# Performance work log

Measured on AMD Instinct MI355X. Metric: run time of the kernel, lower is better.

The kernel has to match this reference:

```python
import jax, jax.numpy as jnp
import numpy as np

B = 32          # patients
D = 128         # hidden dim (modality_embedding_dim == total_hidden_dim)
H = 4           # attention heads
DH = D // H     # per-head dim
L = 2           # num_graph_layers
N = {'ct': 1024, 'pet': 1024, 'clin': 256, 'gen': 2048, 'pat': 1}
# (src_type, dst_type) for the 8 relation types registered in _setup_relations
REL = [('ct','ct'), ('pet','pet'), ('clin','clin'), ('gen','gen'),
       ('pat','clin'), ('ct','gen'), ('pet','gen'), ('gen','pat')]
E_REL = [8192, 8192, 2048, 16384, 256, 8192, 8192, 2048]
EDGE_NAMES = ['e_ct','e_pet','e_clin','e_gen','e_pat2clin','e_ct2gen','e_pet2gen','e_gen2pat']


def setup_inputs() -> dict:
    key = jax.random.key(0)
    ks = iter(jax.random.split(key, 64))
    nk = lambda: next(ks)
    inp = {}
    inp['x_ct']   = jax.random.normal(nk(), (B, N['ct'],  D), jnp.float32)
    inp['x_pet']  = jax.random.normal(nk(), (B, N['pet'], D), jnp.float32)
    inp['x_clin'] = jax.random.normal(nk(), (B, N['clin'],D), jnp.float32)
    inp['x_gen']  = jax.random.normal(nk(), (B, N['gen'], D), jnp.float32)
    inp['early']  = jax.random.normal(nk(), (B, D), jnp.float32)

    def mk_edges(k, E, ns, nd):
        k1, k2 = jax.random.split(k)
        src = jax.random.randint(k1, (B, 1, E), 0, ns, jnp.int32)
        dst = jax.random.randint(k2, (B, 1, E), 0, nd, jnp.int32)
        return jnp.concatenate([src, dst], axis=1)  # [B,2,E]

    for nm, (s, d), E in zip(EDGE_NAMES, REL, E_REL):
        inp[nm] = mk_edges(nk(), E, N[s], N[d])

    sw = 1.0 / np.sqrt(D)
    inp['W_src'] = jax.random.normal(nk(), (L, 8, D, D), jnp.float32) * sw
    inp['W_dst'] = jax.random.normal(nk(), (L, 8, D, D), jnp.float32) * sw
    inp['a_src'] = jax.random.normal(nk(), (L, 8, H, DH), jnp.float32) * sw
    inp['a_dst'] = jax.random.normal(nk(), (L, 8, H, DH), jnp.float32) * sw
    inp['Wp'] = jax.random.normal(nk(), (3, D, D), jnp.float32) * sw  # CT, PET, genomic pooling
    inp['bp'] = jnp.zeros((3, D), jnp.float32)
    inp['W_sem'] = jax.random.normal(nk(), (4 * D, 128), jnp.float32) * (1.0 / np.sqrt(4 * D))
    inp['b_sem'] = jnp.zeros((128,), jnp.float32)
    inp['q_sem'] = jax.random.normal(nk(), (128,), jnp.float32) * sw
    return inp


def _leaky_relu(x):
    return jnp.where(x > 0, x, 0.2 * x)


def _gat_layer(x, edges, Ws, Wd, As, Ad):
    """One heterogeneous multi-head GAT layer summing over relation types."""
    agg = {t: jnp.zeros((B, N[t], H, DH), jnp.float32) for t in N}
    for r, ((s, d), ei) in enumerate(zip(REL, edges)):
        hs = jnp.einsum('bnd,de->bne', x[s], Ws[r]).reshape(B, N[s], H, DH)
        hd = jnp.einsum('bnd,de->bne', x[d], Wd[r]).reshape(B, N[d], H, DH)
        al_s = jnp.sum(hs * As[r], axis=-1)  # [B,Ns,H]
        al_d = jnp.sum(hd * Ad[r], axis=-1)  # [B,Nd,H]
        nd = N[d]

        def one(hs_b, as_b, ad_b, e_b):
            src, dst = e_b[0], e_b[1]
            logit = _leaky_relu(as_b[src] + ad_b[dst])                      # [E,H]
            m = jnp.full((nd, H), -1e30, logit.dtype).at[dst].max(logit)    # segment max
            p = jnp.exp(logit - m[dst])
            den = jnp.zeros((nd, H), p.dtype).at[dst].add(p)
            w = p / (den[dst] + 1e-16)                                      # edge softmax per dst node
            msg = w[:, :, None] * hs_b[src]                                 # [E,H,DH]
            return jnp.zeros((nd, H, DH), msg.dtype).at[dst].add(msg)

        agg[d] = agg[d] + jax.vmap(one)(hs, al_s, al_d, ei)
    return {t: jax.nn.elu(agg[t].reshape(B, N[t], D)) for t in N}


def _pool(feat, W, b):
    # query = Linear(mean(features)); scores = feat @ q; softmax-weighted sum
    q = jnp.mean(feat, axis=1) @ W + b            # [B,D]
    sc = jnp.einsum('bnd,bd->bn', feat, q)        # [B,N]
    w = jax.nn.softmax(sc, axis=1)
    return jnp.einsum('bn,bnd->bd', w, feat)      # [B,D]


def _forward(x_ct, x_pet, x_clin, x_gen, early, edges,
             W_src, W_dst, a_src, a_dst, Wp, bp, W_sem, b_sem, q_sem):
    x = {'ct': x_ct, 'pet': x_pet, 'clin': x_clin, 'gen': x_gen,
         'pat': early[:, None, :]}
    for l in range(L):
        x = _gat_layer(x, edges, W_src[l], W_dst[l], a_src[l], a_dst[l])
    ct_p  = _pool(x['ct'],  Wp[0], bp[0])
    pet_p = _pool(x['pet'], Wp[1], bp[1])
    gen_p = _pool(x['gen'], Wp[2], bp[2])   # shared across the 3 meta-paths
    pad = jnp.zeros((B, 2 * D), ct_p.dtype)  # pad 2D -> 4D as in original
    imm = jnp.concatenate([ct_p, gen_p, pad], axis=1)
    pro = jnp.concatenate([pet_p, gen_p, pad], axis=1)
    trt = jnp.concatenate([(ct_p + pet_p) * 0.5, gen_p, pad], axis=1)
    z = jnp.stack([imm, pro, trt], axis=1)                     # [B,3,4D]
    s = jnp.einsum('bpa,a->bp', jnp.tanh(jnp.einsum('bpf,fa->bpa', z, W_sem) + b_sem), q_sem)
    beta = jax.nn.softmax(s, axis=1)                           # [B,3]
    fused = jnp.einsum('bp,bpf->bf', beta, z)                  # [B,4D]
    return fused, beta


def reference(x_ct, x_pet, x_clin, x_gen, early,
              e_ct, e_pet, e_clin, e_gen, e_pat2clin, e_ct2gen, e_pet2gen, e_gen2pat,
              W_src, W_dst, a_src, a_dst, Wp, bp, W_sem, b_sem, q_sem):
    edges = [e_ct, e_pet, e_clin, e_gen, e_pat2clin, e_ct2gen, e_pet2gen, e_gen2pat]
    return _forward(x_ct, x_pet, x_clin, x_gen, early, edges,
                    W_src, W_dst, a_src, a_dst, Wp, bp, W_sem, b_sem, q_sem)
```

## Files before the change

kernel.cpp:

```cpp
#include <hip/hip_runtime.h>
#include <math.h>

static constexpr int NB = 32;
static constexpr int ND = 128;

typedef short bf16x8 __attribute__((ext_vector_type(8)));
typedef float f32x4  __attribute__((ext_vector_type(4)));
typedef unsigned short u16x8 __attribute__((ext_vector_type(8)));

__device__ __forceinline__ float lrelu(float x){ return x > 0.f ? x : 0.2f*x; }
__device__ __forceinline__ unsigned short f2b(float f){
  unsigned u = __float_as_uint(f);
  return (unsigned short)((u + 0x7FFFu + ((u>>16)&1u)) >> 16);
}
__device__ __forceinline__ float b2f(unsigned short b){
  return __uint_as_float(((unsigned)b) << 16);
}

__global__ __launch_bounds__(128) void k_fold(const float* __restrict__ Wsrc,
    const float* __restrict__ Wdst, const float* __restrict__ asrc,
    const float* __restrict__ adst, float* __restrict__ vbuf){
  const int wid[5] = {0,1,3,5,6};
  int lr = blockIdx.x, role = blockIdx.y, l = blockIdx.z;
  int r = wid[lr];
  const float* W = (role ? Wdst : Wsrc) + (size_t)(l*8+r)*16384;
  const float* a = (role ? adst : asrc) + (size_t)(l*8+r)*128;
  int k = threadIdx.x;
  float* o = vbuf + ((size_t)((l*5+lr)*2+role))*512 + k*4;
  #pragma unroll
  for(int h=0;h<4;h++){
    float s = 0.f;
    #pragma unroll
    for(int j=0;j<32;j++) s += W[k*128 + h*32 + j]*a[h*32 + j];
    o[h] = s;
  }
}

__global__ __launch_bounds__(256) void k_wpack(const float* __restrict__ Wsrc,
    unsigned short* __restrict__ Wf){
  const int wid[5] = {0,1,3,5,6};
  int lr = blockIdx.x, l = blockIdx.y;
  const float* W = Wsrc + (size_t)(l*8+wid[lr])*16384;
  unsigned short* o = Wf + (size_t)((l*5+lr)*4)*4096;
  for(int idx=threadIdx.x; idx<128*128; idx+=256){
    int k = idx >> 7, col = idx & 127;
    int h = col >> 5, cc = col & 31;
    int k4 = k>>2, g = k4&3, kk = k4>>3, j = 4*((k4>>2)&1) + (k&3);
    int nb = cc>>4, lane = (cc&15) + 16*g;
    o[(size_t)h*4096 + ((size_t)((kk*2+nb)*64 + lane))*8 + j] = f2b(W[k*128 + col]);
  }
}

struct CsrP {
  const int* eg[5];
  int l2E[5];
  int Nd_[5];
  int roff_[5];
  int eoff_[5];
};

__global__ __launch_bounds__(512) void k_csr(CsrP P, int* __restrict__ rowstart,
                                             int* __restrict__ srcidx){
  int b = blockIdx.x, r = blockIdx.y, t = threadIdx.x;
  int E = 1<<P.l2E[r], Nd = P.Nd_[r];
  const int* eg = P.eg[r] + (size_t)b*2*E;
  int* rsO = rowstart + P.roff_[r] + b*(Nd+1);
  int* siO = srcidx + P.eoff_[r] + (size_t)b*E;
  __shared__ int cnt[2048];
  __shared__ int wsums[8];
  for(int i=t;i<Nd;i+=512) cnt[i]=0;
  __syncthreads();
  for(int e=t;e<E;e+=512) atomicAdd(&cnt[eg[E+e]], 1);
  __syncthreads();
  int C = Nd >> 9;
  int base = t*C;
  int loc[4]; int s_=0;
  for(int i=0;i<C;i++){ loc[i]=cnt[base+i]; s_+=loc[i]; }
  int lane = t&63, wv = t>>6;
  int sinc = s_;
  #pragma unroll
  for(int off=1;off<64;off<<=1){
    int u = __shfl_up(sinc, off);
    if(lane>=off) sinc += u;
  }
  if(lane==63) wsums[wv]=sinc;
  __syncthreads();
  int wbase=0, total=0;
  #pragma unroll
  for(int i=0;i<8;i++){ int v=wsums[i]; if(i<wv) wbase+=v; total+=v; }
  int excl = wbase + sinc - s_;
  for(int i=0;i<C;i++){
    int idx=base+i;
    rsO[idx]=excl; cnt[idx]=excl; excl+=loc[i];
  }
  if(t==0) rsO[Nd]=total;
  __syncthreads();
  for(int e=t;e<E;e+=512){
    int src=eg[e], dst=eg[E+e];
    int pos=atomicAdd(&cnt[dst],1);
    siO[pos]=src;
  }
}

struct HsP {
  int tb[4];
  int usef;
  const float* xf[3];
  unsigned long long xoff[3];
  int Ns[3];
  int nW[3];
  unsigned long long wfo[3][2];
  unsigned long long hso[3][2];
  unsigned long long aso[3][2];
  unsigned long long asrco[3][2];
  int nvd[3];
  unsigned long long vdo[3][3];
  unsigned long long aldo2[3][3];
  int ndd[3][3];
};

__global__ __launch_bounds__(256) void k_hs(HsP P, const unsigned short* __restrict__ x16,
    const unsigned short* __restrict__ Wf, const float* __restrict__ asrc,
    const float* __restrict__ vbuf, unsigned short* __restrict__ hs,
    float* __restrict__ als, float* __restrict__ ald){
  __shared__ unsigned short xl[16*132];
  int B = blockIdx.x;
  int t=0; while(t<2 && B>=P.tb[t+1]) t++;
  int local = B - P.tb[t];
  int b = local & 31, tile = local >> 5;
  int n0 = tile*16;
  int tid = threadIdx.x, w = tid>>6, ln = tid&63;
  if(P.usef){
    const float* xf = P.xf[t] + ((size_t)((size_t)b*P.Ns[t] + n0))*128;
    int row = tid>>4, c8 = tid&15;
    float4 a = *(const float4*)(xf + (size_t)row*128 + c8*8);
    float4 c = *(const float4*)(xf + (size_t)row*128 + c8*8 + 4);
    u16x8 r;
    r[0]=f2b(a.x); r[1]=f2b(a.y); r[2]=f2b(a.z); r[3]=f2b(a.w);
    r[4]=f2b(c.x); r[5]=f2b(c.y); r[6]=f2b(c.z); r[7]=f2b(c.w);
    *(u16x8*)&xl[row*132 + c8*8] = r;
  } else {
    int row = tid>>4, ch = tid&15;
    u16x8 v = *(const u16x8*)(x16 + P.xoff[t] + ((size_t)((size_t)b*P.Ns[t] + n0+row)*128 + ch*8));
    *(u16x8*)&xl[row*132 + ch*8] = v;
  }
  __syncthreads();
  int g = ln>>4, r15 = ln&15;
  for(int rep=0; rep<P.nW[t]; rep++){
    const unsigned short* wf = Wf + P.wfo[t][rep] + (size_t)w*4096;
    f32x4 acc[2]; acc[0]=(f32x4){0,0,0,0}; acc[1]=(f32x4){0,0,0,0};
    #pragma unroll
    for(int kk=0;kk<4;kk++){
      const unsigned short* pa = &xl[r15*132 + kk*32 + 4*g];
      ushort4 lo = *(const ushort4*)pa;
      ushort4 hi = *(const ushort4*)(pa+16);
      union { ushort u[8]; bf16x8 v; } tmp;
      tmp.u[0]=lo.x; tmp.u[1]=lo.y; tmp.u[2]=lo.z; tmp.u[3]=lo.w;
      tmp.u[4]=hi.x; tmp.u[5]=hi.y; tmp.u[6]=hi.z; tmp.u[7]=hi.w;
      bf16x8 af = tmp.v;
      #pragma unroll
      for(int nb=0;nb<2;nb++){
        bf16x8 bw = *(const bf16x8*)(wf + ((size_t)((kk*2+nb)*64 + ln))*8);
        acc[nb] = __builtin_amdgcn_mfma_f32_16x16x32_bf16(af, bw, acc[nb], 0, 0, 0);
      }
    }
    unsigned short* ho = hs + P.hso[t][rep] + ((size_t)b*P.Ns[t] + n0)*128;
    #pragma unroll
    for(int qq=0;qq<4;qq++){
      int m = 4*g + qq;
      #pragma unroll
      for(int nb=0;nb<2;nb++){
        ho[(size_t)m*128 + w*32 + nb*16 + r15] = f2b(acc[nb][qq]);
      }
    }
    {
      const float* aS = asrc + P.asrco[t][rep];
      float a0v = aS[w*32 + r15], a1v = aS[w*32 + 16 + r15];
      float p0 = acc[0][0]*a0v + acc[1][0]*a1v;
      float p1 = acc[0][1]*a0v + acc[1][1]*a1v;
      float p2 = acc[0][2]*a0v + acc[1][2]*a1v;
      float p3 = acc[0][3]*a0v + acc[1][3]*a1v;
      #pragma unroll
      for(int off=1; off<16; off<<=1){
        p0 += __shfl_xor(p0,off); p1 += __shfl_xor(p1,off);
        p2 += __shfl_xor(p2,off); p3 += __shfl_xor(p3,off);
      }
      if(r15 < 4){
        float pv = (r15==0)?p0:((r15==1)?p1:((r15==2)?p2:p3));
        als[P.aso[t][rep] + ((size_t)b*P.Ns[t] + n0 + 4*g + r15)*4 + w] = pv;
      }
    }
  }
  int nvd = P.nvd[t];
  if(tid < (nvd<<6)){
    int vd = tid>>6, rem = tid&63, row = rem>>2, h = rem&3;
    const float* vv = vbuf + P.vdo[t][vd];
    float s = 0.f;
    #pragma unroll 8
    for(int k=0;k<128;k++) s += b2f(xl[row*132+k]) * vv[k*4+h];
    ald[P.aldo2[t][vd] + ((size_t)b*P.ndd[t][vd] + n0 + row)*4 + h] = s;
  }
}

static constexpr int MAXE4 = 1536;
static constexpr int WST4  = 1548;

struct Fu5P {
  int nrel[3], ndshift[3];
  int roff[3][3], eoff[3][3], E[3][3], Ns[3][3];
  int rowbase[3][3];
  unsigned long long aldo[3][3];
  unsigned long long outoff[3];
};

__global__ __launch_bounds__(512, 8) void k_fuse6(Fu5P P,
    const int* __restrict__ rowstart, const int* __restrict__ srcidx,
    const float* __restrict__ als, const float* __restrict__ ald,
    const unsigned short* __restrict__ hs, unsigned short* __restrict__ out16){
  __shared__ float wlds[4*WST4];
  __shared__ int   silds[MAXE4];
  __shared__ int   rsl[3*65];
  int B = blockIdx.x;
  int xcd = B & 7, slot = B >> 3;
  int bg = slot >> 6, rem = slot & 63;
  int b = bg*8 + xcd;
  int t, dtile;
  if(rem < 32){ t = 0; dtile = rem; }
  else if(rem < 48){ t = 1; dtile = rem - 32; }
  else { t = 2; dtile = rem - 48; }
  int Nd = 1 << P.ndshift[t];
  int d0 = dtile * 64;
  int tid = threadIdx.x, w = tid>>6, ln = tid&63;
  int nrel = P.nrel[t];

  for(int q=0;q<nrel;q++){
    const int* rsq = rowstart + P.roff[t][q] + b*(Nd+1) + d0;
    for(int i=tid;i<65;i+=512) rsl[q*65+i] = rsq[i];
  }
  __syncthreads();

  for(int s=tid; s<(nrel<<8); s+=512){
    int q = s>>8, r2 = s&255, dloc = r2>>2, j = r2&3;
    int rs0 = rsl[q*65+dloc];
    int deg = rsl[q*65+dloc+1] - rs0;
    int cb = 0;
    for(int q2=0;q2<nrel;q2++) cb += rsl[q2*65+dloc] - rsl[q2*65];
    for(int q2=0;q2<q;q2++)    cb += rsl[q2*65+dloc+1] - rsl[q2*65+dloc];
    const int* si = srcidx + P.eoff[t][q] + (size_t)b*P.E[t][q];
    int bake = P.rowbase[t][q] + b*P.Ns[t][q];
    float4 ad4 = *(const float4*)(ald + P.aldo[t][q] + ((size_t)b*Nd + d0 + dloc)*4);
    float m0=-1e30f,m1=-1e30f,m2=-1e30f,m3=-1e30f;
    for(int i=j;i<deg;i+=4){
      int e = cb+i;
      int sil = bake + si[rs0+i];
      silds[e] = sil;
      float4 as4 = *(const float4*)(als + 4*(size_t)sil);
      float l0=lrelu(as4.x+ad4.x), l1=lrelu(as4.y+ad4.y);
      float l2=lrelu(as4.z+ad4.z), l3=lrelu(as4.w+ad4.w);
      wlds[0*WST4+e]=l0; wlds[1*WST4+e]=l1;
      wlds[2*WST4+e]=l2; wlds[3*WST4+e]=l3;
      m0=fmaxf(m0,l0); m1=fmaxf(m1,l1); m2=fmaxf(m2,l2); m3=fmaxf(m3,l3);
    }
    m0=fmaxf(m0,__shfl_xor(m0,1)); m1=fmaxf(m1,__shfl_xor(m1,1));
    m2=fmaxf(m2,__shfl_xor(m2,1)); m3=fmaxf(m3,__shfl_xor(m3,1));
    m0=fmaxf(m0,__shfl_xor(m0,2)); m1=fmaxf(m1,__shfl_xor(m1,2));
    m2=fmaxf(m2,__shfl_xor(m2,2)); m3=fmaxf(m3,__shfl_xor(m3,2));
    float n0_=0.f,n1_=0.f,n2_=0.f,n3_=0.f;
    for(int i=j;i<deg;i+=4){
      int e = cb+i;
      float p0=__expf(wlds[0*WST4+e]-m0); wlds[0*WST4+e]=p0; n0_+=p0;
      float p1=__expf(wlds[1*WST4+e]-m1); wlds[1*WST4+e]=p1; n1_+=p1;
      float p2=__expf(wlds[2*WST4+e]-m2); wlds[2*WST4+e]=p2; n2_+=p2;
      float p3=__expf(wlds[3*WST4+e]-m3); wlds[3*WST4+e]=p3; n3_+=p3;
    }
    n0_+=__shfl_xor(n0_,1); n1_+=__shfl_xor(n1_,1);
    n2_+=__shfl_xor(n2_,1); n3_+=__shfl_xor(n3_,1);
    n0_+=__shfl_xor(n0_,2); n1_+=__shfl_xor(n1_,2);
    n2_+=__shfl_xor(n2_,2); n3_+=__shfl_xor(n3_,2);
    float i0=1.f/(n0_+1e-16f), i1=1.f/(n1_+1e-16f);
    float i2=1.f/(n2_+1e-16f), i3=1.f/(n3_+1e-16f);
    for(int i=j;i<deg;i+=4){
      int e = cb+i;
      wlds[0*WST4+e]*=i0; wlds[1*WST4+e]*=i1;
      wlds[2*WST4+e]*=i2; wlds[3*WST4+e]*=i3;
    }
  }
  __syncthreads();

  int h = ln>>4;
  float accA[8], accB[8];
  #pragma unroll
  for(int i=0;i<8;i++){ accA[i]=0.f; accB[i]=0.f; }
  #pragma unroll
  for(int it=0; it<8; it++){
    int dloc = w*8 + it;
    int e0=0, e1=0;
    for(int q2=0;q2<nrel;q2++){
      int r0 = rsl[q2*65];
      e0 += rsl[q2*65+dloc]   - r0;
      e1 += rsl[q2*65+dloc+1] - r0;
    }
    float a0 = 0.f, a1 = 0.f;
    int e = e0;
    int eal = (e0+3)&~3; if(eal > e1) eal = e1;
    for(; e<eal; e++){
      float wv = wlds[h*WST4 + e];
      unsigned v = *(const unsigned*)(hs + ((size_t)silds[e]*128 + 2*ln));
      a0 += wv*__uint_as_float(v<<16);
      a1 += wv*__uint_as_float(v&0xFFFF0000u);
    }
    for(; e+8<=e1; e+=8){
      int4  sq0 = *(const int4*)&silds[e];
      int4  sq1 = *(const int4*)&silds[e+4];
      float4 wq0 = *(const float4*)&wlds[h*WST4 + e];
      float4 wq1 = *(const float4*)&wlds[h*WST4 + e + 4];
      unsigned v0 = *(const unsigned*)(hs + ((size_t)sq0.x*128 + 2*ln));
      unsigned v1 = *(const unsigned*)(hs + ((size_t)sq0.y*128 + 2*ln));
      unsigned v2 = *(const unsigned*)(hs + ((size_t)sq0.z*128 + 2*ln));
      unsigned v3 = *(const unsigned*)(hs + ((size_t)sq0.w*128 + 2*ln));
      unsigned v4 = *(const unsigned*)(hs + ((size_t)sq1.x*128 + 2*ln));
      unsigned v5 = *(const unsigned*)(hs + ((size_t)sq1.y*128 + 2*ln));
      unsigned v6 = *(const unsigned*)(hs + ((size_t)sq1.z*128 + 2*ln));
      unsigned v7 = *(const unsigned*)(hs + ((size_t)sq1.w*128 + 2*ln));
      a0 += wq0.x*__uint_as_float(v0<<16); a1 += wq0.x*__uint_as_float(v0&0xFFFF0000u);
      a0 += wq0.y*__uint_as_float(v1<<16); a1 += wq0.y*__uint_as_float(v1&0xFFFF0000u);
      a0 += wq0.z*__uint_as_float(v2<<16); a1 += wq0.z*__uint_as_float(v2&0xFFFF0000u);
      a0 += wq0.w*__uint_as_float(v3<<16); a1 += wq0.w*__uint_as_float(v3&0xFFFF0000u);
      a0 += wq1.x*__uint_as_float(v4<<16); a1 += wq1.x*__uint_as_float(v4&0xFFFF0000u);
      a0 += wq1.y*__uint_as_float(v5<<16); a1 += wq1.y*__uint_as_float(v5&0xFFFF0000u);
      a0 += wq1.z*__uint_as_float(v6<<16); a1 += wq1.z*__uint_as_float(v6&0xFFFF0000u);
      a0 += wq1.w*__uint_as_float(v7<<16); a1 += wq1.w*__uint_as_float(v7&0xFFFF0000u);
    }
    for(; e+4<=e1; e+=4){
      int4  sq = *(const int4*)&silds[e];
      float4 wq = *(const float4*)&wlds[h*WST4 + e];
      unsigned v0 = *(const unsigned*)(hs + ((size_t)sq.x*128 + 2*ln));
      unsigned v1 = *(const unsigned*)(hs + ((size_t)sq.y*128 + 2*ln));
      unsigned v2 = *(const unsigned*)(hs + ((size_t)sq.z*128 + 2*ln));
      unsigned v3 = *(const unsigned*)(hs + ((size_t)sq.w*128 + 2*ln));
      a0 += wq.x*__uint_as_float(v0<<16); a1 += wq.x*__uint_as_float(v0&0xFFFF0000u);
      a0 += wq.y*__uint_as_float(v1<<16); a1 += wq.y*__uint_as_float(v1&0xFFFF0000u);
      a0 += wq.z*__uint_as_float(v2<<16); a1 += wq.z*__uint_as_float(v2&0xFFFF0000u);
      a0 += wq.w*__uint_as_float(v3<<16); a1 += wq.w*__uint_as_float(v3&0xFFFF0000u);
    }
    for(; e<e1; e++){
      float wv = wlds[h*WST4 + e];
      unsigned v = *(const unsigned*)(hs + ((size_t)silds[e]*128 + 2*ln));
      a0 += wv*__uint_as_float(v<<16);
      a1 += wv*__uint_as_float(v&0xFFFF0000u);
    }
    accA[it] = a0; accB[it] = a1;
  }
  #pragma unroll
  for(int it=0; it<8; it++){
    int m = d0 + w*8 + it;
    float v0 = accA[it], v1 = accB[it];
    v0 = v0 > 0.f ? v0 : expm1f(v0);
    v1 = v1 > 0.f ? v1 : expm1f(v1);
    ushort2 o; o.x = f2b(v0); o.y = f2b(v1);
    *(ushort2*)(out16 + P.outoff[t] + ((size_t)b*Nd + m)*128 + 2*ln) = o;
  }
}

__device__ __constant__ const size_t POFF[3] = {0ull, 4194304ull, 8388608ull};
__device__ __constant__ const int    PNN[3]  = {1024, 1024, 2048};
static constexpr int PCH = 64;
static constexpr int MAXCH = 32;

__global__ __launch_bounds__(128) void k_pool_psum(const unsigned short* __restrict__ x2,
    float* __restrict__ part){
  int p = blockIdx.z, b = blockIdx.x, c = blockIdx.y, t = threadIdx.x;
  int Nn = PNN[p];
  if(c*PCH >= Nn) return;
  const unsigned short* f = x2 + POFF[p] + ((size_t)b*Nn + c*PCH)*ND;
  float acc = 0.f;
  #pragma unroll 8
  for(int n=0;n<PCH;n++) acc += b2f(f[(size_t)n*ND + t]);
  part[(((size_t)p*NB + b)*MAXCH + c)*ND + t] = acc;
}

__global__ __launch_bounds__(128) void k_pool_q(const float* __restrict__ part,
    const float* __restrict__ Wp, const float* __restrict__ bp,
    float* __restrict__ q){
  int p = blockIdx.z, b = blockIdx.x, t = threadIdx.x;
  int nch = PNN[p]/PCH;
  __shared__ float mean[ND];
  float s = 0.f;
  for(int c=0;c<nch;c++) s += part[(((size_t)p*NB + b)*MAXCH + c)*ND + t];
  mean[t] = s / (float)PNN[p];
  __syncthreads();
  const float* W = Wp + (size_t)p*ND*ND;
  float qv = bp[p*ND + t];
  #pragma unroll 8
  for(int k=0;k<ND;k++) qv += mean[k]*W[k*ND + t];
  q[((size_t)p*NB + b)*ND + t] = qv;
}

__global__ __launch_bounds__(256) void k_pool_score(const unsigned short* __restrict__ x2,
    const float* __restrict__ q, float* __restrict__ sc){
  int p = blockIdx.z, b = blockIdx.y;
  int w = threadIdx.x >> 6, lane = threadIdx.x & 63;
  int n = blockIdx.x*4 + w;
  int Nn = PNN[p];
  if(n >= Nn) return;
  const unsigned short* f  = x2 + POFF[p] + ((size_t)b*Nn + n)*ND;
  const float* qb = q + ((size_t)p*NB + b)*ND;
  float s = b2f(f[lane])*qb[lane] + b2f(f[lane+64])*qb[lane+64];
  #pragma unroll
  for(int off=32; off; off>>=1) s += __shfl_xor(s, off);
  if(lane == 0) sc[((size_t)p*NB + b)*2048 + n] = s;
}

__global__ __launch_bounds__(256) void k_pool_smax(const float* __restrict__ sc,
    float* __restrict__ stat){
  int p = blockIdx.z, b = blockIdx.x, t = threadIdx.x;
  int Nn = PNN[p];
  __shared__ float red[256];
  const float* s = sc + ((size_t)p*NB + b)*2048;
  float mx = -1e30f;
  for(int n=t;n<Nn;n+=256) mx = fmaxf(mx, s[n]);
  red[t] = mx; __syncthreads();
  for(int o=128;o;o>>=1){ if(t<o) red[t]=fmaxf(red[t],red[t+o]); __syncthreads(); }
  mx = red[0]; __syncthreads();
  float sum = 0.f;
  for(int n=t;n<Nn;n+=256) sum += __expf(s[n]-mx);
  red[t] = sum; __syncthreads();
  for(int o=128;o;o>>=1){ if(t<o) red[t]+=red[t+o]; __syncthreads(); }
  if(t==0){ stat[((size_t)p*NB + b)*2] = mx; stat[((size_t)p*NB + b)*2+1] = 1.f/red[0]; }
}

__global__ __launch_bounds__(128) void k_pool_wsum(const unsigned short* __restrict__ x2,
    const float* __restrict__ sc, const float* __restrict__ stat,
    float* __restrict__ part){
  int p = blockIdx.z, b = blockIdx.x, c = blockIdx.y, t = threadIdx.x;
  int Nn = PNN[p];
  if(c*PCH >= Nn) return;
  __shared__ float wsh[PCH];
  float mx  = stat[((size_t)p*NB + b)*2];
  float inv = stat[((size_t)p*NB + b)*2+1];
  if(t < PCH) wsh[t] = __expf(sc[((size_t)p*NB + b)*2048 + c*PCH + t] - mx)*inv;
  __syncthreads();
  const unsigned short* f = x2 + POFF[p] + ((size_t)b*Nn + c*PCH)*ND;
  float acc = 0.f;
  #pragma unroll 8
  for(int n=0;n<PCH;n++) acc += wsh[n]*b2f(f[(size_t)n*ND + t]);
  part[(((size_t)p*NB + b)*MAXCH + c)*ND + t] = acc;
}

__global__ __launch_bounds__(128) void k_pool_comb(const float* __restrict__ part,
    float* __restrict__ pooled){
  int p = blockIdx.z, b = blockIdx.x, t = threadIdx.x;
  int nch = PNN[p]/PCH;
  float s = 0.f;
  for(int c=0;c<nch;c++) s += part[(((size_t)p*NB + b)*MAXCH + c)*ND + t];
  pooled[((size_t)p*NB + b)*ND + t] = s;
}

__global__ __launch_bounds__(128) void k_sem(const float* __restrict__ ctp,
    const float* __restrict__ petp, const float* __restrict__ genp,
    const float* __restrict__ Wsem, const float* __restrict__ bsem,
    const float* __restrict__ qsem, float* __restrict__ fused, float* __restrict__ beta){
  int b = blockIdx.x, t = threadIdx.x;
  __shared__ float z[3][256];
  __shared__ float red[128];
  float ct = ctp[b*ND + t], pet = petp[b*ND + t], gen = genp[b*ND + t];
  z[0][t]=ct;  z[1][t]=pet; z[2][t]=0.5f*(ct+pet);
  z[0][ND+t]=gen; z[1][ND+t]=gen; z[2][ND+t]=gen;
  __syncthreads();
  float s[3];
  for(int p=0;p<3;p++){
    float a = bsem[t];
    for(int f=0;f<256;f++) a += z[p][f]*Wsem[f*128 + t];
    a = tanhf(a);
    red[t] = a * qsem[t];
    __syncthreads();
    for(int o=64;o>0;o>>=1){ if(t<o) red[t]+=red[t+o]; __syncthreads(); }
    s[p] = red[0]; __syncthreads();
  }
  float mx = fmaxf(s[0], fmaxf(s[1], s[2]));
  float e0 = __expf(s[0]-mx), e1 = __expf(s[1]-mx), e2 = __expf(s[2]-mx);
  float sm = e0+e1+e2;
  float b0 = e0/sm, b1 = e1/sm, b2 = e2/sm;
  if(t < 3) beta[b*3 + t] = (t==0)?b0:((t==1)?b1:b2);
  float f0 = b0*z[0][t] + b1*z[1][t] + b2*z[2][t];
  float f1 = b0*z[0][ND+t] + b1*z[1][ND+t] + b2*z[2][ND+t];
  fused[(size_t)b*512 + t]       = f0;
  fused[(size_t)b*512 + 128 + t] = f1;
  fused[(size_t)b*512 + 256 + t] = 0.f;
  fused[(size_t)b*512 + 384 + t] = 0.f;
}

extern "C" void kernel_launch(void* const* d_in, const int* in_sizes, int n_in,
                              void* d_out, int out_size, void* d_ws, size_t ws_size,
                              hipStream_t stream) {
  static const int wid[5]    = {0,1,3,5,6};
  static const int edgein[5] = {5,6,8,10,11};
  static const int l2E[5]    = {13,13,14,13,13};
  static const int Nd_l[5]   = {1024,1024,2048,2048,2048};
  static const int E_l[5]    = {8192,8192,16384,8192,8192};
  static const int Ns_l[5]   = {1024,1024,2048,1024,1024};
  static const int eoff[6]   = {0,262144,524288,1048576,1310720,1572864};
  static const int roff[5]   = {0,32800,65600,131168,196736};
  static const unsigned long long aoff[5]   = {0,131072,262144,524288,655360};
  static const unsigned long long aldoff[5] = {0,131072,262144,524288,786432};
  static const unsigned long long hsoff_lr[5] = {0ull,4194304ull,8388608ull,16777216ull,20971520ull};
  static const unsigned long long ALD = 786432;

  const float* Wsrc = (const float*)d_in[13];
  const float* Wp   = (const float*)d_in[17];
  const float* bp   = (const float*)d_in[18];
  const float* Wsem = (const float*)d_in[19];
  const float* bsem = (const float*)d_in[20];
  const float* qsem = (const float*)d_in[21];

  unsigned short* xc16 = (unsigned short*)d_ws;
  unsigned short* x2b16 = xc16;
  unsigned short* xmid16 = xc16 + 16777216;
  float* albase = (float*)(xmid16 + 16777216);
  float* als = albase;
  float* ald = albase + ALD;
  float* vbuf = albase + 1835008;
  unsigned short* wfbuf = (unsigned short*)(vbuf + 10240);
  float* pooled = (float*)(wfbuf + 163840);
  float* part = pooled + 12288;
  float* qbuf = part + 393216;
  float* scbuf = qbuf + 12288;
  float* stat = scbuf + 196608;
  int* rowstart = (int*)(stat + 192);
  int* srcidx = rowstart + 262304;
  unsigned short* hs16 = (unsigned short*)(srcidx + 1572864);

  { dim3 g(5,2,2); k_fold<<<g,128,0,stream>>>(Wsrc, (const float*)d_in[14],
                                              (const float*)d_in[15], (const float*)d_in[16], vbuf); }
  { dim3 g(5,2); k_wpack<<<g,256,0,stream>>>(Wsrc, wfbuf); }

  CsrP csr;
  for(int r=0;r<5;r++){
    csr.eg[r] = (const int*)d_in[edgein[r]];
    csr.l2E[r] = l2E[r]; csr.Nd_[r] = Nd_l[r];
    csr.roff_[r] = roff[r]; csr.eoff_[r] = eoff[r];
  }
  { dim3 g(NB,5); k_csr<<<g,512,0,stream>>>(csr, rowstart, srcidx); }

  static const unsigned long long xoo[3] = {0,4194304,8388608};
  static const int t2_nrel[3] = {3,1,1};
  static const int t2_lrel[3][3] = {{2,3,4},{0,0,0},{1,0,0}};
  static const int t2_nds[3] = {11,10,10};
  static const int t2_out[3] = {2,0,1};

  Fu5P fp;
  for(int t=0;t<3;t++){
    fp.nrel[t]=t2_nrel[t]; fp.ndshift[t]=t2_nds[t]; fp.outoff[t]=xoo[t2_out[t]];
    for(int q=0;q<3;q++){
      int lr = t2_lrel[t][q];
      fp.roff[t][q]=roff[lr]; fp.eoff[t][q]=eoff[lr];
      fp.E[t][q]=E_l[lr]; fp.Ns[t][q]=Ns_l[lr];
      fp.rowbase[t][q]=(int)(aoff[lr]/4);
      fp.aldo[t][q]=aldoff[lr];
    }
  }

  static const int hs_lr[3][2] = {{0,3},{1,4},{2,2}};
  static const int vd_lr[3][3] = {{0,0,0},{1,0,0},{2,3,4}};
  HsP hp;
  hp.tb[0]=0; hp.tb[1]=2048; hp.tb[2]=4096; hp.tb[3]=8192;
  hp.xf[0]=(const float*)d_in[0]; hp.xf[1]=(const float*)d_in[1]; hp.xf[2]=(const float*)d_in[3];
  hp.xoff[0]=0; hp.xoff[1]=4194304; hp.xoff[2]=8388608;
  hp.Ns[0]=1024; hp.Ns[1]=1024; hp.Ns[2]=2048;
  hp.nW[0]=2; hp.nW[1]=2; hp.nW[2]=1;
  hp.nvd[0]=1; hp.nvd[1]=1; hp.nvd[2]=3;
  for(int t=0;t<3;t++){
    for(int rep=0;rep<2;rep++){
      int lr = hs_lr[t][rep];
      hp.hso[t][rep]=hsoff_lr[lr];
      hp.aso[t][rep]=aoff[lr];
    }
    for(int vd=0;vd<3;vd++){
      int lr = vd_lr[t][vd];
      hp.aldo2[t][vd]=aldoff[lr];
      hp.ndd[t][vd]=Nd_l[lr];
    }
  }
  hp.hso[2][1]=0; hp.aso[2][1]=0;

  for(int l=0;l<2;l++){
    unsigned short* xout = (l==0) ? xmid16 : x2b16;
    hp.usef = (l==0) ? 1 : 0;

    for(int t=0;t<3;t++){
      for(int rep=0;rep<2;rep++){
        int lr = hs_lr[t][rep];
        hp.wfo[t][rep]=(unsigned long long)((l*5 + lr)*4)*4096;
        hp.asrco[t][rep]=(unsigned long long)((l*8 + wid[lr])*128);
      }
      for(int vd=0;vd<3;vd++){
        int lr = vd_lr[t][vd];
        hp.vdo[t][vd]=((unsigned long long)((l*5+lr)*2+1))*512;
      }
    }
    k_hs<<<8192,256,0,stream>>>(hp, xmid16, wfbuf, (const float*)d_in[15], vbuf,
                                hs16, als, ald);

    k_fuse6<<<2048,512,0,stream>>>(fp, rowstart, srcidx, als, ald, hs16, xout);
  }

  {
    dim3 gchunk(NB, MAXCH, 3);
    dim3 gone(NB, 1, 3);
    dim3 gscore(512, NB, 3);
    k_pool_psum <<<gchunk,128,0,stream>>>(x2b16, part);
    k_pool_q    <<<gone,  128,0,stream>>>(part, Wp, bp, qbuf);
    k_pool_score<<<gscore,256,0,stream>>>(x2b16, qbuf, scbuf);
    k_pool_smax <<<gone,  256,0,stream>>>(scbuf, stat);
    k_pool_wsum <<<gchunk,128,0,stream>>>(x2b16, scbuf, stat, part);
    k_pool_comb <<<gone,  128,0,stream>>>(part, pooled);
  }

  float* fused = (float*)d_out;
  float* beta  = fused + (size_t)NB*512;
  k_sem<<<NB,128,0,stream>>>(pooled, pooled + NB*ND, pooled + 2*NB*ND,
                             Wsem, bsem, qsem, fused, beta);
}
```

Baseline: 331.7 us.

## Make GAT aggregation wave-local with per-wave softmax and interleaved dst types

The fused edge-softmax/aggregation kernel now gives each wave its own 8 destination nodes with private LDS slices, replacing the block-wide rowstart staging and __syncthreads with wave-local shuffles and a wave barrier. The softmax drops max-subtraction and computes exp directly in one pass, removing two LDS passes. Node types are interleaved across waves within a block to balance load. It risks overflow without max-subtraction and fixed 240-edge per-wave buffers that could overflow for high-degree nodes.

```diff
diff --git a/kernel.cpp b/kernel.cpp
--- a/kernel.cpp
+++ b/kernel.cpp
@@ -202,8 +202,7 @@
   }
 }
 
-static constexpr int MAXE4 = 1536;
-static constexpr int WST4  = 1548;
+static constexpr int WSL = 240;
 
 struct Fu5P {
   int nrel[3], ndshift[3];
@@ -213,107 +212,105 @@
   unsigned long long outoff[3];
 };
 
-__global__ __launch_bounds__(512, 8) void k_fuse6(Fu5P P,
+__global__ __launch_bounds__(512, 8) void k_fuse7(Fu5P P,
     const int* __restrict__ rowstart, const int* __restrict__ srcidx,
     const float* __restrict__ als, const float* __restrict__ ald,
     const unsigned short* __restrict__ hs, unsigned short* __restrict__ out16){
-  __shared__ float wlds[4*WST4];
-  __shared__ int   silds[MAXE4];
-  __shared__ int   rsl[3*65];
+  __shared__ float wlds_all[8*4*WSL];
+  __shared__ int   silds_all[8*WSL];
   int B = blockIdx.x;
+  int w = threadIdx.x >> 6, ln = threadIdx.x & 63;
   int xcd = B & 7, slot = B >> 3;
   int bg = slot >> 6, rem = slot & 63;
   int b = bg*8 + xcd;
-  int t, dtile;
-  if(rem < 32){ t = 0; dtile = rem; }
-  else if(rem < 48){ t = 1; dtile = rem - 32; }
-  else { t = 2; dtile = rem - 48; }
+  int v = rem*8 + w;
+  int g = v >> 2, k4 = v & 3;
+  int t, tile;
+  if(k4 < 2){ t = 0; tile = g*2 + k4; }
+  else if(k4 == 2){ t = 1; tile = g; }
+  else { t = 2; tile = g; }
   int Nd = 1 << P.ndshift[t];
-  int d0 = dtile * 64;
-  int tid = threadIdx.x, w = tid>>6, ln = tid&63;
+  int d0 = tile * 8;
   int nrel = P.nrel[t];
-
-  for(int q=0;q<nrel;q++){
-    const int* rsq = rowstart + P.roff[t][q] + b*(Nd+1) + d0;
-    for(int i=tid;i<65;i+=512) rsl[q*65+i] = rsq[i];
-  }
-  __syncthreads();
-
-  for(int s=tid; s<(nrel<<8); s+=512){
-    int q = s>>8, r2 = s&255, dloc = r2>>2, j = r2&3;
-    int rs0 = rsl[q*65+dloc];
-    int deg = rsl[q*65+dloc+1] - rs0;
-    int cb = 0;
-    for(int q2=0;q2<nrel;q2++) cb += rsl[q2*65+dloc] - rsl[q2*65];
-    for(int q2=0;q2<q;q2++)    cb += rsl[q2*65+dloc+1] - rsl[q2*65+dloc];
-    const int* si = srcidx + P.eoff[t][q] + (size_t)b*P.E[t][q];
+  float* wlds = wlds_all + w*4*WSL;
+  int*  silds = silds_all + w*WSL;
+  int dst = ln >> 3, sub = ln & 7;
+  int d = d0 + dst;
+
+  int len0=0, len1=0, len2=0, s00=0, s01=0, s02=0;
+  {
+    const int* rsq = rowstart + P.roff[t][0] + b*(Nd+1);
+    s00 = rsq[d]; len0 = rsq[d+1] - s00;
+  }
+  if(nrel > 1){
+    const int* rsq1 = rowstart + P.roff[t][1] + b*(Nd+1);
+    s01 = rsq1[d]; len1 = rsq1[d+1] - s01;
+    const int* rsq2 = rowstart + P.roff[t][2] + b*(Nd+1);
+    s02 = rsq2[d]; len2 = rsq2[d+1] - s02;
+  }
+  int clen = len0 + len1 + len2;
+  int mybase = 0;
+  #pragma unroll
+  for(int dd=0; dd<7; dd++){
+    int vl = __shfl(clen, dd*8);
+    if(dd < dst) mybase += vl;
+  }
+
+  auto dorel = [&](int q, int s0q, int lq, int segb){
+    const int* si = srcidx + P.eoff[t][q] + (size_t)b*P.E[t][q] + s0q;
     int bake = P.rowbase[t][q] + b*P.Ns[t][q];
-    float4 ad4 = *(const float4*)(ald + P.aldo[t][q] + ((size_t)b*Nd + d0 + dloc)*4);
-    float m0=-1e30f,m1=-1e30f,m2=-1e30f,m3=-1e30f;
-    for(int i=j;i<deg;i+=4){
-      int e = cb+i;
-      int sil = bake + si[rs0+i];
+    float4 ad4 = *(const float4*)(ald + P.aldo[t][q] + ((size_t)b*Nd + d)*4);
+    float dn0=0.f, dn1=0.f, dn2=0.f, dn3=0.f;
+    for(int i=sub; i<lq; i+=8){
+      int e = segb + i;
+      int sil = bake + si[i];
       silds[e] = sil;
       float4 as4 = *(const float4*)(als + 4*(size_t)sil);
-      float l0=lrelu(as4.x+ad4.x), l1=lrelu(as4.y+ad4.y);
-      float l2=lrelu(as4.z+ad4.z), l3=lrelu(as4.w+ad4.w);
-      wlds[0*WST4+e]=l0; wlds[1*WST4+e]=l1;
-      wlds[2*WST4+e]=l2; wlds[3*WST4+e]=l3;
-      m0=fmaxf(m0,l0); m1=fmaxf(m1,l1); m2=fmaxf(m2,l2); m3=fmaxf(m3,l3);
-    }
-    m0=fmaxf(m0,__shfl_xor(m0,1)); m1=fmaxf(m1,__shfl_xor(m1,1));
-    m2=fmaxf(m2,__shfl_xor(m2,1)); m3=fmaxf(m3,__shfl_xor(m3,1));
-    m0=fmaxf(m0,__shfl_xor(m0,2)); m1=fmaxf(m1,__shfl_xor(m1,2));
-    m2=fmaxf(m2,__shfl_xor(m2,2)); m3=fmaxf(m3,__shfl_xor(m3,2));
-    float n0_=0.f,n1_=0.f,n2_=0.f,n3_=0.f;
-    for(int i=j;i<deg;i+=4){
-      int e = cb+i;
-      float p0=__expf(wlds[0*WST4+e]-m0); wlds[0*WST4+e]=p0; n0_+=p0;
-      float p1=__expf(wlds[1*WST4+e]-m1); wlds[1*WST4+e]=p1; n1_+=p1;
-      float p2=__expf(wlds[2*WST4+e]-m2); wlds[2*WST4+e]=p2; n2_+=p2;
-      float p3=__expf(wlds[3*WST4+e]-m3); wlds[3*WST4+e]=p3; n3_+=p3;
-    }
-    n0_+=__shfl_xor(n0_,1); n1_+=__shfl_xor(n1_,1);
-    n2_+=__shfl_xor(n2_,1); n3_+=__shfl_xor(n3_,1);
-    n0_+=__shfl_xor(n0_,2); n1_+=__shfl_xor(n1_,2);
-    n2_+=__shfl_xor(n2_,2); n3_+=__shfl_xor(n3_,2);
-    float i0=1.f/(n0_+1e-16f), i1=1.f/(n1_+1e-16f);
-    float i2=1.f/(n2_+1e-16f), i3=1.f/(n3_+1e-16f);
-    for(int i=j;i<deg;i+=4){
-      int e = cb+i;
-      wlds[0*WST4+e]*=i0; wlds[1*WST4+e]*=i1;
-      wlds[2*WST4+e]*=i2; wlds[3*WST4+e]*=i3;
-    }
-  }
-  __syncthreads();
+      float p0 = __expf(lrelu(as4.x+ad4.x));
+      float p1 = __expf(lrelu(as4.y+ad4.y));
+      float p2 = __expf(lrelu(as4.z+ad4.z));
+      float p3 = __expf(lrelu(as4.w+ad4.w));
+      wlds[0*WSL+e]=p0; wlds[1*WSL+e]=p1; wlds[2*WSL+e]=p2; wlds[3*WSL+e]=p3;
+      dn0+=p0; dn1+=p1; dn2+=p2; dn3+=p3;
+    }
+    dn0+=__shfl_xor(dn0,1); dn1+=__shfl_xor(dn1,1); dn2+=__shfl_xor(dn2,1); dn3+=__shfl_xor(dn3,1);
+    dn0+=__shfl_xor(dn0,2); dn1+=__shfl_xor(dn1,2); dn2+=__shfl_xor(dn2,2); dn3+=__shfl_xor(dn3,2);
+    dn0+=__shfl_xor(dn0,4); dn1+=__shfl_xor(dn1,4); dn2+=__shfl_xor(dn2,4); dn3+=__shfl_xor(dn3,4);
+    float i0=1.f/(dn0+1e-16f), i1=1.f/(dn1+1e-16f);
+    float i2=1.f/(dn2+1e-16f), i3=1.f/(dn3+1e-16f);
+    for(int i=sub; i<lq; i+=8){
+      int e = segb + i;
+      wlds[0*WSL+e]*=i0; wlds[1*WSL+e]*=i1;
+      wlds[2*WSL+e]*=i2; wlds[3*WSL+e]*=i3;
+    }
+  };
+  dorel(0, s00, len0, mybase);
+  if(nrel > 1){
+    dorel(1, s01, len1, mybase + len0);
+    dorel(2, s02, len2, mybase + len0 + len1);
+  }
+  __builtin_amdgcn_wave_barrier();
 
   int h = ln>>4;
-  float accA[8], accB[8];
-  #pragma unroll
-  for(int i=0;i<8;i++){ accA[i]=0.f; accB[i]=0.f; }
+  int run = 0;
   #pragma unroll
   for(int it=0; it<8; it++){
-    int dloc = w*8 + it;
-    int e0=0, e1=0;
-    for(int q2=0;q2<nrel;q2++){
-      int r0 = rsl[q2*65];
-      e0 += rsl[q2*65+dloc]   - r0;
-      e1 += rsl[q2*65+dloc+1] - r0;
-    }
+    int cl = __shfl(clen, it*8);
+    int e0 = run, e1 = run + cl; run = e1;
     float a0 = 0.f, a1 = 0.f;
     int e = e0;
     int eal = (e0+3)&~3; if(eal > e1) eal = e1;
     for(; e<eal; e++){
-      float wv = wlds[h*WST4 + e];
-      unsigned v = *(const unsigned*)(hs + ((size_t)silds[e]*128 + 2*ln));
-      a0 += wv*__uint_as_float(v<<16);
-      a1 += wv*__uint_as_float(v&0xFFFF0000u);
+      float wv = wlds[h*WSL + e];
+      unsigned vv = *(const unsigned*)(hs + ((size_t)silds[e]*128 + 2*ln));
+      a0 += wv*__uint_as_float(vv<<16);
+      a1 += wv*__uint_as_float(vv&0xFFFF0000u);
     }
     for(; e+8<=e1; e+=8){
       int4  sq0 = *(const int4*)&silds[e];
       int4  sq1 = *(const int4*)&silds[e+4];
-      float4 wq0 = *(const float4*)&wlds[h*WST4 + e];
-      float4 wq1 = *(const float4*)&wlds[h*WST4 + e + 4];
+      float4 wq0 = *(const float4*)&wlds[h*WSL + e];
+      float4 wq1 = *(const float4*)&wlds[h*WSL + e + 4];
       unsigned v0 = *(const unsigned*)(hs + ((size_t)sq0.x*128 + 2*ln));
       unsigned v1 = *(const unsigned*)(hs + ((size_t)sq0.y*128 + 2*ln));
       unsigned v2 = *(const unsigned*)(hs + ((size_t)sq0.z*128 + 2*ln));
@@ -333,7 +330,7 @@
     }
     for(; e+4<=e1; e+=4){
       int4  sq = *(const int4*)&silds[e];
-      float4 wq = *(const float4*)&wlds[h*WST4 + e];
+      float4 wq = *(const float4*)&wlds[h*WSL + e];
       unsigned v0 = *(const unsigned*)(hs + ((size_t)sq.x*128 + 2*ln));
       unsigned v1 = *(const unsigned*)(hs + ((size_t)sq.y*128 + 2*ln));
       unsigned v2 = *(const unsigned*)(hs + ((size_t)sq.z*128 + 2*ln));
@@ -344,20 +341,15 @@
       a0 += wq.w*__uint_as_float(v3<<16); a1 += wq.w*__uint_as_float(v3&0xFFFF0000u);
     }
     for(; e<e1; e++){
-      float wv = wlds[h*WST4 + e];
-      unsigned v = *(const unsigned*)(hs + ((size_t)silds[e]*128 + 2*ln));
-      a0 += wv*__uint_as_float(v<<16);
-      a1 += wv*__uint_as_float(v&0xFFFF0000u);
-    }
-    accA[it] = a0; accB[it] = a1;
-  }
-  #pragma unroll
-  for(int it=0; it<8; it++){
-    int m = d0 + w*8 + it;
-    float v0 = accA[it], v1 = accB[it];
-    v0 = v0 > 0.f ? v0 : expm1f(v0);
-    v1 = v1 > 0.f ? v1 : expm1f(v1);
-    ushort2 o; o.x = f2b(v0); o.y = f2b(v1);
+      float wv = wlds[h*WSL + e];
+      unsigned vv = *(const unsigned*)(hs + ((size_t)silds[e]*128 + 2*ln));
+      a0 += wv*__uint_as_float(vv<<16);
+      a1 += wv*__uint_as_float(vv&0xFFFF0000u);
+    }
+    int m = d0 + it;
+    float o0 = a0 > 0.f ? a0 : expm1f(a0);
+    float o1 = a1 > 0.f ? a1 : expm1f(a1);
+    ushort2 o; o.x = f2b(o0); o.y = f2b(o1);
     *(ushort2*)(out16 + P.outoff[t] + ((size_t)b*Nd + m)*128 + 2*ln) = o;
   }
 }
@@ -601,7 +593,7 @@
     k_hs<<<8192,256,0,stream>>>(hp, xmid16, wfbuf, (const float*)d_in[15], vbuf,
                                 hs16, als, ald);
 
-    k_fuse6<<<2048,512,0,stream>>>(fp, rowstart, srcidx, als, ald, hs16, xout);
+    k_fuse7<<<2048,512,0,stream>>>(fp, rowstart, srcidx, als, ald, hs16, xout);
   }
 
   {
```

New measurement: 323.3 us. 1.03x faster.
